# Kernel optimization log

Measured on AMD Instinct MI355X. Metric: run time of the kernel, lower is better.

## Reference

```python
import jax, jax.numpy as jnp
import numpy as np

HID = 2048
HEADS = 16
HD = HID // HEADS  # 128


def setup_inputs() -> dict:
    key = jax.random.key(0)
    ks = jax.random.split(key, 9)
    s = 0.02
    return {
        "hidden_state": jax.random.normal(ks[0], (2, 2048, HID), dtype=jnp.float32),
        "Wq": jax.random.normal(ks[1], (HID, HID), dtype=jnp.float32) * s,
        "bq": jnp.zeros((HID,), dtype=jnp.float32),
        "Wk": jax.random.normal(ks[2], (HID, HD), dtype=jnp.float32) * s,
        "bk": jnp.zeros((HD,), dtype=jnp.float32),
        "Wv": jax.random.normal(ks[3], (HID, HD), dtype=jnp.float32) * s,
        "bv": jnp.zeros((HD,), dtype=jnp.float32),
        "Wo": jax.random.normal(ks[4], (HID, HID), dtype=jnp.float32) * s,
        "bo": jnp.zeros((HID,), dtype=jnp.float32),
    }


def reference(hidden_state, Wq, bq, Wk, bk, Wv, bv, Wo, bo):
    bs, seq, _ = hidden_state.shape
    # Q: [b, s, H, hd] -> per-head; K,V: single shared head [b, s, hd]
    q = (hidden_state @ Wq + bq).reshape(bs, seq, HEADS, HD)
    k = hidden_state @ Wk + bk  # [b, s, hd]
    v = hidden_state @ Wv + bv  # [b, s, hd]
    scale = 1.0 / jnp.sqrt(jnp.float32(HD))
    # scores: [b, h, s_q, s_k] against shared K head
    scores = jnp.einsum("bqhd,bkd->bhqk", q, k) * scale
    attn = jax.nn.softmax(scores, axis=-1)
    out = jnp.einsum("bhqk,bkd->bqhd", attn, v)  # [b, s, h, hd]
    out = out.reshape(bs, seq, HID)
    return out @ Wo + bo
```

## Files before the change

### kernel.cpp

```cpp
#include <hip/hip_runtime.h>
#include <math.h>

#define HIDN 2048
#define NHEADS 16
#define HDIM 128
#define SEQ 2048
#define NB 2

#define C2 0.12751744154f

typedef __bf16 bf16x8 __attribute__((ext_vector_type(8)));
typedef float f32x4 __attribute__((ext_vector_type(4)));

__device__ __forceinline__ unsigned short f32_to_bf16(float f) {
  unsigned int u = __float_as_uint(f);
  u += 0x7FFFu + ((u >> 16) & 1u);
  return (unsigned short)(u >> 16);
}

__device__ __forceinline__ unsigned pack_bf16x2(float a, float b) {
  return (unsigned)f32_to_bf16(a) | ((unsigned)f32_to_bf16(b) << 16);
}

__device__ __forceinline__ unsigned pack_bf16x2_trunc(float a, float b) {
  return __builtin_amdgcn_perm(__float_as_uint(b), __float_as_uint(a), 0x07060302u);
}

__device__ __forceinline__ void gload_lds16(const void* g, void* l) {
  __builtin_amdgcn_global_load_lds(
      (__attribute__((address_space(1))) void*)(g),
      (__attribute__((address_space(3))) void*)(l), 16, 0, 0);
}

__global__ __launch_bounds__(256) void prep(
    const float* __restrict__ hidden, unsigned short* __restrict__ hb,
    const float* __restrict__ wq, unsigned short* __restrict__ dq,
    const float* __restrict__ wo, unsigned short* __restrict__ do_,
    const float* __restrict__ wk, const float* __restrict__ wv,
    unsigned short* __restrict__ dk, unsigned short* __restrict__ dv,
    const float* __restrict__ bq, const float* __restrict__ bk,
    const float* __restrict__ bv, float* __restrict__ biasout) {
  __shared__ float tile[32][33];
  const int blk = blockIdx.x;
  const int tx = threadIdx.x & 31, ty = threadIdx.x >> 5;
  if (blk < 8192) {
    int i = blk * 256 + threadIdx.x;
    float4 v = ((const float4*)hidden)[i];
    ushort4 o;
    o.x = f32_to_bf16(v.x); o.y = f32_to_bf16(v.y);
    o.z = f32_to_bf16(v.z); o.w = f32_to_bf16(v.w);
    ((ushort4*)hb)[i] = o;
    return;
  }
  if (blk < 16384) {
    int r = blk - 8192;
    const int z = r >> 12; r &= 4095;
    const int bx = r & 63, by = r >> 6;
    const float* src = z ? wo : wq;
    unsigned short* dst = z ? do_ : dq;
    const float m = z ? 1.0f : C2;
    const int c0 = bx * 32, r0 = by * 32;
#pragma unroll
    for (int i = 0; i < 32; i += 8)
      tile[ty + i][tx] = src[(size_t)(r0 + ty + i) * 2048 + c0 + tx];
    __syncthreads();
#pragma unroll
    for (int i = 0; i < 32; i += 8)
      dst[(size_t)(c0 + ty + i) * 2048 + r0 + tx] = f32_to_bf16(tile[tx][ty + i] * m);
    return;
  }
  {
    int r = blk - 16384;
    const int z = r >> 8; r &= 255;
    const int bx = r & 3, by = r >> 2;
    const float* src = z ? wv : wk;
    unsigned short* dst = z ? dv : dk;
    const int c0 = bx * 32, r0 = by * 32;
#pragma unroll
    for (int i = 0; i < 32; i += 8)
      tile[ty + i][tx] = src[(size_t)(r0 + ty + i) * 128 + c0 + tx];
    __syncthreads();
#pragma unroll
    for (int i = 0; i < 32; i += 8)
      dst[(size_t)(c0 + ty + i) * 2048 + r0 + tx] = f32_to_bf16(tile[tx][ty + i]);
    if (z == 0) {
      int lb = by * 4 + bx;
      if (lb < 9) {
        int i = lb * 256 + threadIdx.x;
        if (i < 2304)
          biasout[i] = (i < 2048) ? bq[i] * C2
                                  : ((i < 2176) ? bk[i - 2048] : bv[i - 2176]);
      }
    }
  }
}

__global__ __launch_bounds__(256) void vtrans(
    const unsigned short* __restrict__ qkv, unsigned short* __restrict__ vt) {
  __shared__ unsigned short tile[32][33];
  const unsigned short* src = qkv + (size_t)blockIdx.z * SEQ * 2304 + 2176;
  unsigned short* dst = vt + (size_t)blockIdx.z * 128 * SEQ;
  int c0 = blockIdx.x * 32, r0 = blockIdx.y * 32;
  int tx = threadIdx.x & 31, ty = threadIdx.x >> 5;
#pragma unroll
  for (int i = 0; i < 32; i += 8)
    tile[ty + i][tx] = src[(size_t)(r0 + ty + i) * 2304 + c0 + tx];
  __syncthreads();
  const int s = r0 + tx;
  const int col = (s & ~63) | (((s >> 5) & 1) * 32 + ((s >> 2) & 3) * 8 +
                               ((s >> 4) & 1) * 4 + (s & 3));
#pragma unroll
  for (int i = 0; i < 32; i += 8)
    dst[(size_t)(c0 + ty + i) * SEQ + col] = tile[tx][ty + i];
}

template <int BN>
__global__ __launch_bounds__(256) void gemm_bt(
    const unsigned short* __restrict__ A,
    const unsigned short* __restrict__ BT,
    const float* __restrict__ bias,
    void* __restrict__ C, int K, int ldc, int outBf16) {
  constexpr int NT = BN / 32;
  __shared__ unsigned short As[128 * 64];
  __shared__ unsigned short Bs[BN * 64];
  const int tid = threadIdx.x;
  const int lane = tid & 63;
  const int wave = tid >> 6;
  const int wr = wave >> 1, wc = wave & 1;
  const int ml = lane & 15, quad = lane >> 4;
  const long bm = (long)blockIdx.x * 128;
  const long bn = (long)blockIdx.y * BN;

  const f32x4 zero4 = {0.f, 0.f, 0.f, 0.f};
  f32x4 acc[4][NT];
#pragma unroll
  for (int mt = 0; mt < 4; ++mt)
#pragma unroll
    for (int nt = 0; nt < NT; ++nt) acc[mt][nt] = zero4;

  const int srow = lane >> 3;
  const int scol = ((lane & 7) ^ srow) * 8;

  for (int k0 = 0; k0 < K; k0 += 64) {
    __syncthreads();
#pragma unroll
    for (int r = 0; r < 4; ++r) {
      const int rowb = r * 32 + wave * 8;
      gload_lds16(A + (bm + rowb + srow) * (long)K + k0 + scol, &As[rowb * 64]);
    }
#pragma unroll
    for (int r = 0; r < NT; ++r) {
      const int rowb = r * 32 + wave * 8;
      gload_lds16(BT + (bn + rowb + srow) * (long)K + k0 + scol, &Bs[rowb * 64]);
    }
    __syncthreads();
#pragma unroll
    for (int kk = 0; kk < 64; kk += 32) {
      const int g0 = (kk >> 3) + quad;
      bf16x8 af[4], bf[NT];
#pragma unroll
      for (int mt = 0; mt < 4; ++mt)
        af[mt] = *(const bf16x8*)&As[(wr * 64 + mt * 16 + ml) * 64 +
                                     ((g0 ^ (ml & 7)) << 3)];
#pragma unroll
      for (int nt = 0; nt < NT; ++nt)
        bf[nt] = *(const bf16x8*)&Bs[(wc * (BN / 2) + nt * 16 + ml) * 64 +
                                     ((g0 ^ (ml & 7)) << 3)];
#pragma unroll
      for (int mt = 0; mt < 4; ++mt)
#pragma unroll
        for (int nt = 0; nt < NT; ++nt)
          acc[mt][nt] = __builtin_amdgcn_mfma_f32_16x16x32_bf16(
              af[mt], bf[nt], acc[mt][nt], 0, 0, 0);
    }
  }

#pragma unroll
  for (int mt = 0; mt < 4; ++mt) {
#pragma unroll
    for (int nt = 0; nt < NT; ++nt) {
      const long col = bn + wc * (BN / 2) + nt * 16 + ml;
      const float bval = bias ? bias[col] : 0.f;
#pragma unroll
      for (int r = 0; r < 4; ++r) {
        const long row = bm + wr * 64 + mt * 16 + quad * 4 + r;
        const float v = acc[mt][nt][r] + bval;
        if (outBf16)
          ((unsigned short*)C)[row * ldc + col] = f32_to_bf16(v);
        else
          ((float*)C)[row * ldc + col] = v;
      }
    }
  }
}

template <int NBY, int LDC, int OUTBF16>
__global__ __launch_bounds__(512, 2) void gemm_ko(
    const unsigned short* __restrict__ A,
    const unsigned short* __restrict__ BT,
    const float* __restrict__ bias,
    void* __restrict__ C, int K) {
  __shared__ unsigned short As[3][128 * 64];
  __shared__ unsigned short Bs[3][256 * 64];
  const int tid = threadIdx.x;
  const int lane = tid & 63;
  const int wave = tid >> 6;
  const int wr = wave >> 2;
  const int wc = wave & 3;
  const int ml = lane & 15, quad = lane >> 4;

  const int orig = blockIdx.x;
  const int qx = gridDim.x >> 3;
  const int lid = (orig & 7) * qx + (orig >> 3);
  const long bm = (long)(lid / NBY) * 128;
  const long bn = (long)(lid % NBY) * 256;

  const int srow = tid >> 3;
  const int scol = ((tid & 7) ^ (srow & 7)) * 8;
  const unsigned short* Ag = A + (bm + srow) * (long)K + scol;
  const unsigned short* Bg = BT + (bn + srow) * (long)K + scol;

  const f32x4 zero4 = {0.f, 0.f, 0.f, 0.f};
  f32x4 acc[4][4];
#pragma unroll
  for (int mt = 0; mt < 4; ++mt)
#pragma unroll
    for (int nt = 0; nt < 4; ++nt) acc[mt][nt] = zero4;

  bf16x8 bfr[4][2];

#define STA(buf, koff, R0) \
  gload_lds16(Ag + (long)(R0) * K + (koff), &As[buf][((R0) + 8 * wave) * 64])
#define STB(buf, koff, R0) \
  gload_lds16(Bg + (long)(R0) * K + (koff), &Bs[buf][((R0) + 8 * wave) * 64])
#define RDA(buf, mt, kk) \
  (*(const bf16x8*)&As[buf][(wr * 64 + (mt) * 16 + ml) * 64 + \
                            ((((kk) * 4 + quad) ^ (ml & 7)) << 3)])
#define RDB(buf, nt, kk) \
  (*(const bf16x8*)&Bs[buf][(wc * 64 + (nt) * 16 + ml) * 64 + \
                            ((((kk) * 4 + quad) ^ (ml & 7)) << 3)])

  STB(0, 0, 0); STB(0, 0, 64); STB(0, 0, 128); STB(0, 0, 192);
  STA(0, 0, 0); STA(0, 0, 64);
  STB(1, 64, 0); STB(1, 64, 64); STB(1, 64, 128); STB(1, 64, 192);
  STA(1, 64, 0); STA(1, 64, 64);
  asm volatile("s_waitcnt vmcnt(6)" ::: "memory");
  __builtin_amdgcn_s_barrier();

  const int NT = K >> 6;
  for (int t = 0; t < NT; ++t) {
    const int buf = t % 3, sb = (t + 2) % 3;
    const long kn = (long)(t + 2) << 6;
    const bool st = (t + 2) < NT;
    __builtin_amdgcn_sched_barrier(0);
    bf16x8 afr[2][2];
#pragma unroll
    for (int nt = 0; nt < 4; ++nt)
#pragma unroll
      for (int kk = 0; kk < 2; ++kk) bfr[nt][kk] = RDB(buf, nt, kk);
#pragma unroll
    for (int j = 0; j < 2; ++j)
#pragma unroll
      for (int kk = 0; kk < 2; ++kk) afr[j][kk] = RDA(buf, j, kk);
    if (st) { STB(sb, kn, 0); STB(sb, kn, 64); STB(sb, kn, 128); STB(sb, kn, 192); }
    __builtin_amdgcn_s_barrier();
    __builtin_amdgcn_s_setprio(1);
#pragma unroll
    for (int j = 0; j < 2; ++j)
#pragma unroll
      for (int nt = 0; nt < 4; ++nt)
#pragma unroll
        for (int kk = 0; kk < 2; ++kk)
          acc[j][nt] = __builtin_amdgcn_mfma_f32_16x16x32_bf16(
              afr[j][kk], bfr[nt][kk], acc[j][nt], 0, 0, 0);
    __builtin_amdgcn_s_setprio(0);
    __builtin_amdgcn_s_barrier();
    __builtin_amdgcn_sched_barrier(0);
#pragma unroll
    for (int j = 0; j < 2; ++j)
#pragma unroll
      for (int kk = 0; kk < 2; ++kk) afr[j][kk] = RDA(buf, 2 + j, kk);
    if (st) {
      STA(sb, kn, 0); STA(sb, kn, 64);
      asm volatile("s_waitcnt vmcnt(6)" ::: "memory");
    } else if (t == NT - 2) {
      asm volatile("s_waitcnt vmcnt(0)" ::: "memory");
    }
    __builtin_amdgcn_s_barrier();
    __builtin_amdgcn_s_setprio(1);
#pragma unroll
    for (int j = 0; j < 2; ++j)
#pragma unroll
      for (int nt = 0; nt < 4; ++nt)
#pragma unroll
        for (int kk = 0; kk < 2; ++kk)
          acc[2 + j][nt] = __builtin_amdgcn_mfma_f32_16x16x32_bf16(
              afr[j][kk], bfr[nt][kk], acc[2 + j][nt], 0, 0, 0);
    __builtin_amdgcn_s_setprio(0);
    __builtin_amdgcn_s_barrier();
  }
#undef STA
#undef STB
#undef RDA
#undef RDB

#pragma unroll
  for (int mt = 0; mt < 4; ++mt) {
#pragma unroll
    for (int nt = 0; nt < 4; ++nt) {
      const long col = bn + wc * 64 + nt * 16 + ml;
      const float bval = bias ? bias[col] : 0.f;
#pragma unroll
      for (int r = 0; r < 4; ++r) {
        const long row = bm + wr * 64 + mt * 16 + quad * 4 + r;
        const float v = acc[mt][nt][r] + bval;
        if (OUTBF16)
          ((unsigned short*)C)[row * LDC + col] = f32_to_bf16(v);
        else
          ((float*)C)[row * LDC + col] = v;
      }
    }
  }
}

__global__ __launch_bounds__(256, 2) void mqa_attn(
    const unsigned short* __restrict__ qkv,
    const unsigned short* __restrict__ vt,
    unsigned short* __restrict__ outp) {
  __shared__ unsigned short Ks[2][64 * 128];
  __shared__ unsigned short VTs[2][128 * 64];

  const int lane = threadIdx.x & 63;
  const int wave = threadIdx.x >> 6;
  const int ml = lane & 15, quad = lane >> 4;
  const int h = blockIdx.y, b = blockIdx.z;
  const long q0 = (long)blockIdx.x * 128;
  const long base = (long)b * SEQ;

  bf16x8 aq[2][4];
#pragma unroll
  for (int n = 0; n < 2; ++n) {
    const unsigned short* qrow =
        qkv + (base + q0 + wave * 32 + n * 16 + ml) * 2304 + h * 128;
#pragma unroll
    for (int ks = 0; ks < 4; ++ks)
      aq[n][ks] = *(const bf16x8*)(qrow + ks * 32 + quad * 8);
  }

  const f32x4 zero4 = {0.f, 0.f, 0.f, 0.f};
  f32x4 o[8][2];
#pragma unroll
  for (int mt2 = 0; mt2 < 8; ++mt2)
#pragma unroll
    for (int n = 0; n < 2; ++n) o[mt2][n] = zero4;
  f32x4 o9[2] = {zero4, zero4};

  bf16x8 ones_af;
  {
    union { unsigned u[4]; bf16x8 v; } cv;
    const unsigned w = (ml == 0) ? 0x3F803F80u : 0u;
    cv.u[0] = w; cv.u[1] = w; cv.u[2] = w; cv.u[3] = w;
    ones_af = cv.v;
  }

  const int srowK = lane >> 4;
  const int scolK = ((lane & 15) ^ (wave * 4 + srowK)) * 8;
  const int srowV = lane >> 3;
  const int scolV = ((lane & 7) ^ srowV) * 8;
  const unsigned short* kp = qkv + (base + srowK) * 2304 + 2048 + scolK;
  const unsigned short* vp = vt + ((long)b * 128 + srowV) * SEQ + scolV;

  auto stage = [&](int buf, int ktn) {
    const unsigned short* kpp = kp + (long)ktn * (64 * 2304);
    const unsigned short* vpp = vp + ktn * 64;
#pragma unroll
    for (int r = 0; r < 4; ++r) {
      const int rowb = r * 16 + wave * 4;
      gload_lds16(kpp + (long)rowb * 2304, &Ks[buf][rowb * 128]);
    }
#pragma unroll
    for (int r = 0; r < 4; ++r) {
      const int rowb = r * 32 + wave * 8;
      gload_lds16(vpp + (long)rowb * SEQ, &VTs[buf][rowb * 64]);
    }
  };

  stage(0, 0);

  for (int kt = 0; kt < SEQ / 64; ++kt) {
    const int cur = kt & 1;
    __syncthreads();
    if (kt < SEQ / 64 - 1) stage(cur ^ 1, kt + 1);

    f32x4 s[4][2];
#pragma unroll
    for (int mt = 0; mt < 4; ++mt)
#pragma unroll
      for (int n = 0; n < 2; ++n) s[mt][n] = zero4;
#pragma unroll
    for (int ks = 0; ks < 4; ++ks) {
#pragma unroll
      for (int mt = 0; mt < 4; ++mt) {
        bf16x8 ak = *(const bf16x8*)&Ks[cur][(mt * 16 + ml) * 128 +
                                            (((ks * 4 + quad) ^ ml) << 3)];
#pragma unroll
        for (int n = 0; n < 2; ++n)
          s[mt][n] = __builtin_amdgcn_mfma_f32_16x16x32_bf16(
              ak, aq[n][ks], s[mt][n], 0, 0, 0);
      }
    }

    unsigned pk[2][4][2];
#pragma unroll
    for (int mt = 0; mt < 4; ++mt)
#pragma unroll
      for (int n = 0; n < 2; ++n) {
        const float p0 = __builtin_amdgcn_exp2f(s[mt][n][0]);
        const float p1 = __builtin_amdgcn_exp2f(s[mt][n][1]);
        const float p2 = __builtin_amdgcn_exp2f(s[mt][n][2]);
        const float p3 = __builtin_amdgcn_exp2f(s[mt][n][3]);
        pk[n][mt][0] = pack_bf16x2_trunc(p0, p1);
        pk[n][mt][1] = pack_bf16x2_trunc(p2, p3);
      }

#pragma unroll
    for (int ks2 = 0; ks2 < 2; ++ks2) {
      bf16x8 bp[2];
#pragma unroll
      for (int n = 0; n < 2; ++n) {
        union { unsigned u[4]; bf16x8 v; } cv;
        cv.u[0] = pk[n][2 * ks2][0];
        cv.u[1] = pk[n][2 * ks2][1];
        cv.u[2] = pk[n][2 * ks2 + 1][0];
        cv.u[3] = pk[n][2 * ks2 + 1][1];
        bp[n] = cv.v;
      }
#pragma unroll
      for (int n = 0; n < 2; ++n)
        o9[n] = __builtin_amdgcn_mfma_f32_16x16x32_bf16(
            ones_af, bp[n], o9[n], 0, 0, 0);
#pragma unroll
      for (int mt2 = 0; mt2 < 8; ++mt2) {
        bf16x8 av = *(const bf16x8*)&VTs[cur][(mt2 * 16 + ml) * 64 +
                                             (((ks2 * 4 + quad) ^ (ml & 7)) << 3)];
#pragma unroll
        for (int n = 0; n < 2; ++n)
          o[mt2][n] = __builtin_amdgcn_mfma_f32_16x16x32_bf16(
              av, bp[n], o[mt2][n], 0, 0, 0);
      }
    }
  }

  float inv[2];
#pragma unroll
  for (int n = 0; n < 2; ++n)
    inv[n] = 1.f / __shfl(o9[n][0], ml);

#pragma unroll
  for (int n = 0; n < 2; ++n) {
    const long row = base + q0 + wave * 32 + n * 16 + ml;
#pragma unroll
    for (int mt2 = 0; mt2 < 8; ++mt2) {
      uint2 w;
      w.x = pack_bf16x2(o[mt2][n][0] * inv[n], o[mt2][n][1] * inv[n]);
      w.y = pack_bf16x2(o[mt2][n][2] * inv[n], o[mt2][n][3] * inv[n]);
      *(uint2*)&outp[row * HIDN + h * HDIM + mt2 * 16 + quad * 4] = w;
    }
  }
}

extern "C" void kernel_launch(void* const* d_in, const int* in_sizes, int n_in,
                              void* d_out, int out_size, void* d_ws, size_t ws_size,
                              hipStream_t stream) {
  const float* hidden = (const float*)d_in[0];
  const float* Wq = (const float*)d_in[1];
  const float* bq = (const float*)d_in[2];
  const float* Wk = (const float*)d_in[3];
  const float* bk = (const float*)d_in[4];
  const float* Wv = (const float*)d_in[5];
  const float* bv = (const float*)d_in[6];
  const float* Wo = (const float*)d_in[7];
  const float* bo = (const float*)d_in[8];
  float* out = (float*)d_out;

  char* ws = (char*)d_ws;
  const size_t MB = 1u << 20;
  unsigned short* hb    = (unsigned short*)(ws);
  unsigned short* attn  = hb;
  unsigned short* wqkvT = (unsigned short*)(ws + 16 * MB);
  unsigned short* woT   = (unsigned short*)(ws + 25 * MB);
  unsigned short* qkv   = (unsigned short*)(ws + 33 * MB);
  unsigned short* vt    = (unsigned short*)(ws + 51 * MB);
  float* biasqkv        = (float*)(ws + 52 * MB);

  prep<<<16896, 256, 0, stream>>>(hidden, hb, Wq, wqkvT, Wo, woT, Wk, Wv,
                                  wqkvT + (size_t)2048 * 2048,
                                  wqkvT + (size_t)2176 * 2048,
                                  bq, bk, bv, biasqkv);

  gemm_bt<96><<<dim3(32, 24), 256, 0, stream>>>(hb, wqkvT, biasqkv, qkv, 2048, 2304, 1);

  vtrans<<<dim3(4, 64, 2), 256, 0, stream>>>(qkv, vt);

  mqa_attn<<<dim3(SEQ / 128, NHEADS, NB), 256, 0, stream>>>(qkv, vt, attn);

  gemm_ko<8, 2048, 0><<<dim3(256), 512, 0, stream>>>(attn, woT, bo, out, 2048);
}
```

Before: 280.5 us.

## Fuse V transpose into a 256x256 QKV GEMM and replace output GEMM

```diff
diff --git a/kernel.cpp b/kernel.cpp
--- a/kernel.cpp
+++ b/kernel.cpp
@@ -95,34 +95,183 @@
   }
 }
 
-__global__ __launch_bounds__(256) void vtrans(
-    const unsigned short* __restrict__ qkv, unsigned short* __restrict__ vt) {
-  __shared__ unsigned short tile[32][33];
-  const unsigned short* src = qkv + (size_t)blockIdx.z * SEQ * 2304 + 2176;
-  unsigned short* dst = vt + (size_t)blockIdx.z * 128 * SEQ;
-  int c0 = blockIdx.x * 32, r0 = blockIdx.y * 32;
-  int tx = threadIdx.x & 31, ty = threadIdx.x >> 5;
-#pragma unroll
-  for (int i = 0; i < 32; i += 8)
-    tile[ty + i][tx] = src[(size_t)(r0 + ty + i) * 2304 + c0 + tx];
-  __syncthreads();
-  const int s = r0 + tx;
-  const int col = (s & ~63) | (((s >> 5) & 1) * 32 + ((s >> 2) & 3) * 8 +
-                               ((s >> 4) & 1) * 4 + (s & 3));
-#pragma unroll
-  for (int i = 0; i < 32; i += 8)
-    dst[(size_t)(c0 + ty + i) * SEQ + col] = tile[tx][ty + i];
+template <int NBY, int LDC, int OUTBF16, int WRITE_VT>
+__global__ __launch_bounds__(512, 2) void gemm256(
+    const unsigned short* __restrict__ A,
+    const unsigned short* __restrict__ BT,
+    const float* __restrict__ bias,
+    void* __restrict__ C, unsigned short* __restrict__ vtout, int K) {
+  __shared__ unsigned short As[2][256 * 64];
+  __shared__ unsigned short Bs[2][256 * 64];
+  const int tid = threadIdx.x;
+  const int lane = tid & 63;
+  const int wave = tid >> 6;
+  const int wr = wave >> 2;
+  const int wc = wave & 3;
+  const int ml = lane & 15, quad = lane >> 4;
+
+  const int orig = blockIdx.x;
+  const int qx = gridDim.x >> 3;
+  const int lid = (orig & 7) * qx + (orig >> 3);
+  const long bm = (long)(lid / NBY) * 256;
+  const long bn = (long)(lid % NBY) * 256;
+
+  const int srow = tid >> 3;
+  const int scol = ((tid & 7) ^ (srow & 7)) * 8;
+  const unsigned short* Ag = A + (bm + srow) * (long)K + scol;
+  const unsigned short* Bg = BT + (bn + srow) * (long)K + scol;
+
+  const f32x4 zero4 = {0.f, 0.f, 0.f, 0.f};
+  f32x4 acc[8][4];
+#pragma unroll
+  for (int mt = 0; mt < 8; ++mt)
+#pragma unroll
+    for (int nt = 0; nt < 4; ++nt) acc[mt][nt] = zero4;
+
+  bf16x8 bfr[4][2];
+
+#define STA(buf, koff, R0) \
+  gload_lds16(Ag + (long)(R0) * K + (koff), &As[buf][((R0) + 8 * wave) * 64])
+#define STB(buf, koff, R0) \
+  gload_lds16(Bg + (long)(R0) * K + (koff), &Bs[buf][((R0) + 8 * wave) * 64])
+#define RDA(buf, mt, kk) \
+  (*(const bf16x8*)&As[buf][(wr * 128 + (mt) * 16 + ml) * 64 + \
+                            ((((kk) * 4 + quad) ^ (ml & 7)) << 3)])
+#define RDB(buf, nt, kk) \
+  (*(const bf16x8*)&Bs[buf][(wc * 64 + (nt) * 16 + ml) * 64 + \
+                            ((((kk) * 4 + quad) ^ (ml & 7)) << 3)])
+
+  STB(0, 0, 0); STB(0, 0, 64); STB(0, 0, 128); STB(0, 0, 192);
+  STA(0, 0, 0); STA(0, 0, 128); STA(0, 0, 64); STA(0, 0, 192);
+  asm volatile("s_waitcnt vmcnt(2)" ::: "memory");
+  __builtin_amdgcn_s_barrier();
+
+  const int NT = K >> 6;
+  for (int t = 0; t < NT - 1; ++t) {
+    const int buf = t & 1, nbuf = buf ^ 1;
+    const long kn = (long)(t + 1) << 6;
+#pragma unroll
+    for (int q = 0; q < 4; ++q) {
+      __builtin_amdgcn_sched_barrier(0);
+      bf16x8 afr[2][2];
+      if (q == 0) {
+#pragma unroll
+        for (int nt = 0; nt < 4; ++nt)
+#pragma unroll
+          for (int kk = 0; kk < 2; ++kk) bfr[nt][kk] = RDB(buf, nt, kk);
+      }
+#pragma unroll
+      for (int j = 0; j < 2; ++j)
+#pragma unroll
+        for (int kk = 0; kk < 2; ++kk) afr[j][kk] = RDA(buf, 2 * q + j, kk);
+      if (q == 0) {
+        STB(nbuf, kn, 0); STB(nbuf, kn, 64); STB(nbuf, kn, 128); STB(nbuf, kn, 192);
+      }
+      if (q == 1) {
+        STA(nbuf, kn, 0); STA(nbuf, kn, 128);
+        asm volatile("s_waitcnt vmcnt(6)" ::: "memory");
+      }
+      if (q == 2) { STA(nbuf, kn, 64); STA(nbuf, kn, 192); }
+      if (q == 3) {
+        asm volatile("s_waitcnt vmcnt(2)" ::: "memory");
+      }
+      __builtin_amdgcn_s_barrier();
+      asm volatile("s_waitcnt lgkmcnt(0)" ::: "memory");
+      __builtin_amdgcn_s_setprio(1);
+#pragma unroll
+      for (int kk = 0; kk < 2; ++kk)
+#pragma unroll
+        for (int j = 0; j < 2; ++j)
+#pragma unroll
+          for (int nt = 0; nt < 4; ++nt)
+            acc[2 * q + j][nt] = __builtin_amdgcn_mfma_f32_16x16x32_bf16(
+                afr[j][kk], bfr[nt][kk], acc[2 * q + j][nt], 0, 0, 0);
+      __builtin_amdgcn_s_setprio(0);
+      __builtin_amdgcn_s_barrier();
+    }
+  }
+
+  {
+    const int buf = (NT - 1) & 1;
+#pragma unroll
+    for (int q = 0; q < 4; ++q) {
+      __builtin_amdgcn_sched_barrier(0);
+      bf16x8 afr[2][2];
+      if (q == 0) {
+#pragma unroll
+        for (int nt = 0; nt < 4; ++nt)
+#pragma unroll
+          for (int kk = 0; kk < 2; ++kk) bfr[nt][kk] = RDB(buf, nt, kk);
+      }
+#pragma unroll
+      for (int j = 0; j < 2; ++j)
+#pragma unroll
+        for (int kk = 0; kk < 2; ++kk) afr[j][kk] = RDA(buf, 2 * q + j, kk);
+      if (q == 1) asm volatile("s_waitcnt vmcnt(0)" ::: "memory");
+      __builtin_amdgcn_s_barrier();
+      asm volatile("s_waitcnt lgkmcnt(0)" ::: "memory");
+      __builtin_amdgcn_s_setprio(1);
+#pragma unroll
+      for (int kk = 0; kk < 2; ++kk)
+#pragma unroll
+        for (int j = 0; j < 2; ++j)
+#pragma unroll
+          for (int nt = 0; nt < 4; ++nt)
+            acc[2 * q + j][nt] = __builtin_amdgcn_mfma_f32_16x16x32_bf16(
+                afr[j][kk], bfr[nt][kk], acc[2 * q + j][nt], 0, 0, 0);
+      __builtin_amdgcn_s_setprio(0);
+      __builtin_amdgcn_s_barrier();
+    }
+  }
+#undef STA
+#undef STB
+#undef RDA
+#undef RDB
+
+#pragma unroll
+  for (int mt = 0; mt < 8; ++mt) {
+#pragma unroll
+    for (int nt = 0; nt < 4; ++nt) {
+      const long col = bn + wc * 64 + nt * 16 + ml;
+      const float bval = bias ? bias[col] : 0.f;
+      float vv[4];
+#pragma unroll
+      for (int r = 0; r < 4; ++r) {
+        const long row = bm + wr * 128 + mt * 16 + quad * 4 + r;
+        const float v = acc[mt][nt][r] + bval;
+        vv[r] = v;
+        if (OUTBF16)
+          ((unsigned short*)C)[row * LDC + col] = f32_to_bf16(v);
+        else
+          ((float*)C)[row * LDC + col] = v;
+      }
+      if (WRITE_VT) {
+        if (col >= 2176) {
+          const long row0 = bm + wr * 128 + mt * 16 + quad * 4;
+          const int b = (int)(row0 >> 11);
+          const int s0 = (int)(row0 & 2047);
+          const int P = (s0 & ~63) | (((s0 >> 5) & 1) * 32 +
+                                      (((s0 >> 2) & 3) * 8) +
+                                      (((s0 >> 4) & 1) * 4));
+          uint2 w;
+          w.x = pack_bf16x2(vv[0], vv[1]);
+          w.y = pack_bf16x2(vv[2], vv[3]);
+          *(uint2*)&vtout[((long)b * 128 + (col - 2176)) * SEQ + P] = w;
+        }
+      }
+    }
+  }
 }
 
 template <int BN>
-__global__ __launch_bounds__(256) void gemm_bt(
+__global__ __launch_bounds__(256) void gemm_btd(
     const unsigned short* __restrict__ A,
     const unsigned short* __restrict__ BT,
     const float* __restrict__ bias,
     void* __restrict__ C, int K, int ldc, int outBf16) {
   constexpr int NT = BN / 32;
-  __shared__ unsigned short As[128 * 64];
-  __shared__ unsigned short Bs[BN * 64];
+  __shared__ unsigned short As[2][128 * 64];
+  __shared__ unsigned short Bs[2][BN * 64];
   const int tid = threadIdx.x;
   const int lane = tid & 63;
   const int wave = tid >> 6;
@@ -141,31 +290,37 @@
   const int srow = lane >> 3;
   const int scol = ((lane & 7) ^ srow) * 8;
 
-  for (int k0 = 0; k0 < K; k0 += 64) {
-    __syncthreads();
+  auto stage = [&](int buf, int k0) {
 #pragma unroll
     for (int r = 0; r < 4; ++r) {
       const int rowb = r * 32 + wave * 8;
-      gload_lds16(A + (bm + rowb + srow) * (long)K + k0 + scol, &As[rowb * 64]);
+      gload_lds16(A + (bm + rowb + srow) * (long)K + k0 + scol, &As[buf][rowb * 64]);
     }
 #pragma unroll
     for (int r = 0; r < NT; ++r) {
       const int rowb = r * 32 + wave * 8;
-      gload_lds16(BT + (bn + rowb + srow) * (long)K + k0 + scol, &Bs[rowb * 64]);
-    }
+      gload_lds16(BT + (bn + rowb + srow) * (long)K + k0 + scol, &Bs[buf][rowb * 64]);
+    }
+  };
+
+  stage(0, 0);
+  const int NTILES = K >> 6;
+  for (int t = 0; t < NTILES; ++t) {
+    const int cur = t & 1;
     __syncthreads();
+    if (t + 1 < NTILES) stage(cur ^ 1, (t + 1) << 6);
 #pragma unroll
     for (int kk = 0; kk < 64; kk += 32) {
       const int g0 = (kk >> 3) + quad;
       bf16x8 af[4], bf[NT];
 #pragma unroll
       for (int mt = 0; mt < 4; ++mt)
-        af[mt] = *(const bf16x8*)&As[(wr * 64 + mt * 16 + ml) * 64 +
-                                     ((g0 ^ (ml & 7)) << 3)];
+        af[mt] = *(const bf16x8*)&As[cur][(wr * 64 + mt * 16 + ml) * 64 +
+                                          ((g0 ^ (ml & 7)) << 3)];
 #pragma unroll
       for (int nt = 0; nt < NT; ++nt)
-        bf[nt] = *(const bf16x8*)&Bs[(wc * (BN / 2) + nt * 16 + ml) * 64 +
-                                     ((g0 ^ (ml & 7)) << 3)];
+        bf[nt] = *(const bf16x8*)&Bs[cur][(wc * (BN / 2) + nt * 16 + ml) * 64 +
+                                          ((g0 ^ (ml & 7)) << 3)];
 #pragma unroll
       for (int mt = 0; mt < 4; ++mt)
 #pragma unroll
@@ -189,135 +344,6 @@
           ((unsigned short*)C)[row * ldc + col] = f32_to_bf16(v);
         else
           ((float*)C)[row * ldc + col] = v;
-      }
-    }
-  }
-}
-
-template <int NBY, int LDC, int OUTBF16>
-__global__ __launch_bounds__(512, 2) void gemm_ko(
-    const unsigned short* __restrict__ A,
-    const unsigned short* __restrict__ BT,
-    const float* __restrict__ bias,
-    void* __restrict__ C, int K) {
-  __shared__ unsigned short As[3][128 * 64];
-  __shared__ unsigned short Bs[3][256 * 64];
-  const int tid = threadIdx.x;
-  const int lane = tid & 63;
-  const int wave = tid >> 6;
-  const int wr = wave >> 2;
-  const int wc = wave & 3;
-  const int ml = lane & 15, quad = lane >> 4;
-
-  const int orig = blockIdx.x;
-  const int qx = gridDim.x >> 3;
-  const int lid = (orig & 7) * qx + (orig >> 3);
-  const long bm = (long)(lid / NBY) * 128;
-  const long bn = (long)(lid % NBY) * 256;
-
-  const int srow = tid >> 3;
-  const int scol = ((tid & 7) ^ (srow & 7)) * 8;
-  const unsigned short* Ag = A + (bm + srow) * (long)K + scol;
-  const unsigned short* Bg = BT + (bn + srow) * (long)K + scol;
-
-  const f32x4 zero4 = {0.f, 0.f, 0.f, 0.f};
-  f32x4 acc[4][4];
-#pragma unroll
-  for (int mt = 0; mt < 4; ++mt)
-#pragma unroll
-    for (int nt = 0; nt < 4; ++nt) acc[mt][nt] = zero4;
-
-  bf16x8 bfr[4][2];
-
-#define STA(buf, koff, R0) \
-  gload_lds16(Ag + (long)(R0) * K + (koff), &As[buf][((R0) + 8 * wave) * 64])
-#define STB(buf, koff, R0) \
-  gload_lds16(Bg + (long)(R0) * K + (koff), &Bs[buf][((R0) + 8 * wave) * 64])
-#define RDA(buf, mt, kk) \
-  (*(const bf16x8*)&As[buf][(wr * 64 + (mt) * 16 + ml) * 64 + \
-                            ((((kk) * 4 + quad) ^ (ml & 7)) << 3)])
-#define RDB(buf, nt, kk) \
-  (*(const bf16x8*)&Bs[buf][(wc * 64 + (nt) * 16 + ml) * 64 + \
-                            ((((kk) * 4 + quad) ^ (ml & 7)) << 3)])
-
-  STB(0, 0, 0); STB(0, 0, 64); STB(0, 0, 128); STB(0, 0, 192);
-  STA(0, 0, 0); STA(0, 0, 64);
-  STB(1, 64, 0); STB(1, 64, 64); STB(1, 64, 128); STB(1, 64, 192);
-  STA(1, 64, 0); STA(1, 64, 64);
-  asm volatile("s_waitcnt vmcnt(6)" ::: "memory");
-  __builtin_amdgcn_s_barrier();
-
-  const int NT = K >> 6;
-  for (int t = 0; t < NT; ++t) {
-    const int buf = t % 3, sb = (t + 2) % 3;
-    const long kn = (long)(t + 2) << 6;
-    const bool st = (t + 2) < NT;
-    __builtin_amdgcn_sched_barrier(0);
-    bf16x8 afr[2][2];
-#pragma unroll
-    for (int nt = 0; nt < 4; ++nt)
-#pragma unroll
-      for (int kk = 0; kk < 2; ++kk) bfr[nt][kk] = RDB(buf, nt, kk);
-#pragma unroll
-    for (int j = 0; j < 2; ++j)
-#pragma unroll
-      for (int kk = 0; kk < 2; ++kk) afr[j][kk] = RDA(buf, j, kk);
-    if (st) { STB(sb, kn, 0); STB(sb, kn, 64); STB(sb, kn, 128); STB(sb, kn, 192); }
-    __builtin_amdgcn_s_barrier();
-    __builtin_amdgcn_s_setprio(1);
-#pragma unroll
-    for (int j = 0; j < 2; ++j)
-#pragma unroll
-      for (int nt = 0; nt < 4; ++nt)
-#pragma unroll
-        for (int kk = 0; kk < 2; ++kk)
-          acc[j][nt] = __builtin_amdgcn_mfma_f32_16x16x32_bf16(
-              afr[j][kk], bfr[nt][kk], acc[j][nt], 0, 0, 0);
-    __builtin_amdgcn_s_setprio(0);
-    __builtin_amdgcn_s_barrier();
-    __builtin_amdgcn_sched_barrier(0);
-#pragma unroll
-    for (int j = 0; j < 2; ++j)
-#pragma unroll
-      for (int kk = 0; kk < 2; ++kk) afr[j][kk] = RDA(buf, 2 + j, kk);
-    if (st) {
-      STA(sb, kn, 0); STA(sb, kn, 64);
-      asm volatile("s_waitcnt vmcnt(6)" ::: "memory");
-    } else if (t == NT - 2) {
-      asm volatile("s_waitcnt vmcnt(0)" ::: "memory");
-    }
-    __builtin_amdgcn_s_barrier();
-    __builtin_amdgcn_s_setprio(1);
-#pragma unroll
-    for (int j = 0; j < 2; ++j)
-#pragma unroll
-      for (int nt = 0; nt < 4; ++nt)
-#pragma unroll
-        for (int kk = 0; kk < 2; ++kk)
-          acc[2 + j][nt] = __builtin_amdgcn_mfma_f32_16x16x32_bf16(
-              afr[j][kk], bfr[nt][kk], acc[2 + j][nt], 0, 0, 0);
-    __builtin_amdgcn_s_setprio(0);
-    __builtin_amdgcn_s_barrier();
-  }
-#undef STA
-#undef STB
-#undef RDA
-#undef RDB
-
-#pragma unroll
-  for (int mt = 0; mt < 4; ++mt) {
-#pragma unroll
-    for (int nt = 0; nt < 4; ++nt) {
-      const long col = bn + wc * 64 + nt * 16 + ml;
-      const float bval = bias ? bias[col] : 0.f;
-#pragma unroll
-      for (int r = 0; r < 4; ++r) {
-        const long row = bm + wr * 64 + mt * 16 + quad * 4 + r;
-        const float v = acc[mt][nt][r] + bval;
-        if (OUTBF16)
-          ((unsigned short*)C)[row * LDC + col] = f32_to_bf16(v);
-        else
-          ((float*)C)[row * LDC + col] = v;
       }
     }
   }
@@ -498,11 +524,11 @@
                                   wqkvT + (size_t)2176 * 2048,
                                   bq, bk, bv, biasqkv);
 
-  gemm_bt<96><<<dim3(32, 24), 256, 0, stream>>>(hb, wqkvT, biasqkv, qkv, 2048, 2304, 1);
-
-  vtrans<<<dim3(4, 64, 2), 256, 0, stream>>>(qkv, vt);
+  gemm256<9, 2304, 1, 1><<<dim3(144), 512, 0, stream>>>(
+      hb, wqkvT, biasqkv, qkv, vt, 2048);
 
   mqa_attn<<<dim3(SEQ / 128, NHEADS, NB), 256, 0, stream>>>(qkv, vt, attn);
 
-  gemm_ko<8, 2048, 0><<<dim3(256), 512, 0, stream>>>(attn, woT, bo, out, 2048);
-}
+  gemm_btd<128><<<dim3(32, 16), 256, 0, stream>>>(
+      attn, woT, bo, out, 2048, 2048, 0);
+}
```

Measured after the change: 289.9 us. 1.03x slower.
